# Optimization experiments

Measured on AMD Instinct MI355X. Metric: run time of the kernel, lower is better.

Reference implementation:

```python
import jax, jax.numpy as jnp
import numpy as np

# ---- straight-through binary quantizers (custom VJP matches torch autograd.Functions) ----
@jax.custom_vjp
def bq(x):
    return jnp.sign(x)
def _bq_fwd(x):
    return jnp.sign(x), x
def _bq_bwd(x, g):
    return (g * ((x > -1.0) & (x < 1.0)).astype(g.dtype),)
bq.defvjp(_bq_fwd, _bq_bwd)

@jax.custom_vjp
def bq_quad(x):
    return jnp.sign(x)
def _bqq_fwd(x):
    return jnp.sign(x), x
def _bqq_bwd(x, g):
    return (jnp.maximum(2.0 - jnp.abs(2.0 * x), 0.0) * g,)
bq_quad.defvjp(_bqq_fwd, _bqq_bwd)

def bilinear(x, W, s, b):
    # BiLinear: row-centered sign weights scaled by learned per-row factor, sign activations
    Wc = W - jnp.mean(W, axis=-1, keepdims=True)
    Wb = s * bq(Wc)                      # (out, in)
    return bq(x) @ Wb.T + b

def selective_scan(u, delta, A, Bs, Cs, D, delta_bias):
    # u, delta: (B,K,Dn,L); A: (K,Dn,N); Bs,Cs: (B,K,N,L); D, delta_bias: (K,Dn)
    Bn, K, Dn, L = u.shape
    N = A.shape[-1]
    delta = jax.nn.softplus(delta + delta_bias[None, :, :, None])
    def step(h, inp):
        ut, dt, Bt, Ct = inp             # (B,K,Dn),(B,K,Dn),(B,K,N),(B,K,N)
        dA = jnp.exp(dt[..., None] * A[None])
        h = dA * h + (dt * ut)[..., None] * Bt[:, :, None, :]
        y = jnp.einsum('bkdn,bkn->bkd', h, Ct)
        return h, y
    h0 = jnp.zeros((Bn, K, Dn, N), u.dtype)
    _, ys = jax.lax.scan(step, h0,
                         (u.transpose(3, 0, 1, 2), delta.transpose(3, 0, 1, 2),
                          Bs.transpose(3, 0, 1, 2), Cs.transpose(3, 0, 1, 2)))
    y = ys.transpose(1, 2, 3, 0)         # (B,K,Dn,L)
    return y + D[None, :, :, None] * u

def _forward(x, W_in, b_in, s_in, move0_b, conv_W, conv_b, rp_b0, prelu_a, rp_b1,
             Wl, bl, sl, Wd, bd, sd, dt_bias, A_logs, Ds, ln_w, ln_b, W_out, b_out, s_out):
    Bn, H, Wi, dm = x.shape
    Dn = conv_W.shape[0]
    K = 4
    N = A_logs.shape[1]
    R = Wd.shape[2]
    L = H * Wi
    xz = bilinear(x, W_in, s_in, b_in)                  # (B,H,W,2*Dn)
    xp, z = jnp.split(xz, 2, axis=-1)
    xc = xp.transpose(0, 3, 1, 2)                       # (B,Dn,H,W)
    # BConv2d: move0 bias -> sign (quad STE) -> binary conv -> RPReLU -> residual
    t = bq_quad(xc + move0_b[None, :, None, None])
    sc = jax.lax.stop_gradient(jnp.mean(jnp.abs(conv_W), axis=(1, 2, 3), keepdims=True))
    cw = jnp.clip(conv_W, -1.0, 1.0)
    Wb = jax.lax.stop_gradient(sc * jnp.sign(conv_W) - cw) + cw
    t = jax.lax.conv_general_dilated(t, Wb, (1, 1), [(1, 1), (1, 1)],
                                     dimension_numbers=('NCHW', 'OIHW', 'NCHW'))
    t = t + conv_b[None, :, None, None]
    t = t + rp_b0[None, :, None, None]
    t = jnp.where(t >= 0, t, prelu_a[None, :, None, None] * t)
    t = t + rp_b1[None, :, None, None] + xc
    xconv = jax.nn.silu(t)
    # 4-direction scan inputs
    x_flat = xconv.reshape(Bn, Dn, L)
    x_tr = xconv.transpose(0, 1, 3, 2).reshape(Bn, Dn, L)
    x_hwwh = jnp.stack([x_flat, x_tr], axis=1)
    xs = jnp.concatenate([x_hwwh, jnp.flip(x_hwwh, axis=-1)], axis=1)   # (B,K,Dn,L)
    # NOTE: torch does .view(B,L,-1) on contiguous (B,Dn,L) slices = raw reshape (not transpose)
    xin = xs.reshape(Bn, K, L, Dn)
    x_dbl = jax.vmap(bilinear, in_axes=(1, 0, 0, 0), out_axes=1)(xin, Wl, sl, bl)  # (B,K,L,R+2N)
    x_dbl = x_dbl.transpose(0, 1, 3, 2)                                 # (B,K,R+2N,L)
    dts_r, Bs, Cs = jnp.split(x_dbl, [R, R + N], axis=2)
    dts_in = dts_r.reshape(Bn, K, L, R)  # raw reshape, matches torch .view
    dts = jax.vmap(bilinear, in_axes=(1, 0, 0, 0), out_axes=1)(dts_in, Wd, sd, bd)  # (B,K,L,Dn)
    dts = dts.transpose(0, 1, 3, 2)                                     # (B,K,Dn,L)
    A = -jnp.exp(A_logs).reshape(K, Dn, N)
    out_y = selective_scan(xs, dts, A, Bs, Cs, Ds.reshape(K, Dn), dt_bias.reshape(K, Dn))
    inv_y = jnp.flip(out_y[:, 2:4], axis=-1)
    wh_y = out_y[:, 1].reshape(Bn, Dn, Wi, H).transpose(0, 1, 3, 2).reshape(Bn, Dn, L)
    invwh_y = inv_y[:, 1].reshape(Bn, Dn, Wi, H).transpose(0, 1, 3, 2).reshape(Bn, Dn, L)
    y = out_y[:, 0] + inv_y[:, 0] + wh_y + invwh_y                      # (B,Dn,L)
    y = y.transpose(0, 2, 1).reshape(Bn, H, Wi, Dn)
    mu = jnp.mean(y, axis=-1, keepdims=True)
    var = jnp.var(y, axis=-1, keepdims=True)
    y = (y - mu) / jnp.sqrt(var + 1e-5) * ln_w + ln_b                   # LayerNorm eps=1e-5
    y = y * jax.nn.silu(z)
    return bilinear(y, W_out, s_out, b_out)

def setup_inputs():
    key = jax.random.key(0)
    ks = jax.random.split(key, 12)
    B, H, Wi, dm = 4, 64, 64, 96
    Dn, N, R, K = 192, 16, 6, 4
    u = lambda k, sh, a: jax.random.uniform(k, sh, jnp.float32, -a, a)
    x = jax.random.normal(ks[0], (B, H, Wi, dm), jnp.float32)
    W_in = u(ks[1], (2 * Dn, dm), 0.015)
    b_in = u(ks[2], (2 * Dn,), 0.01)
    s_in = jnp.mean(jnp.abs(W_in), axis=1, keepdims=True)
    move0_b = jnp.zeros((Dn,), jnp.float32)
    conv_W = 0.05 * jax.random.normal(ks[3], (Dn, Dn, 3, 3), jnp.float32)
    conv_b = u(ks[4], (Dn,), 0.01)
    rp_b0 = jnp.zeros((Dn,), jnp.float32)
    prelu_a = 0.25 * jnp.ones((Dn,), jnp.float32)
    rp_b1 = jnp.zeros((Dn,), jnp.float32)
    Wl = u(ks[5], (K, R + 2 * N, Dn), 0.015)
    bl = u(ks[6], (K, R + 2 * N), 0.01)
    sl = jnp.mean(jnp.abs(Wl), axis=2, keepdims=True)
    std = R ** -0.5
    Wd = u(ks[7], (K, Dn, R), std)
    bd = u(ks[8], (K, Dn), 0.01)
    sd = jnp.mean(jnp.abs(Wd), axis=2, keepdims=True)
    dt = jnp.exp(jax.random.uniform(ks[9], (K * Dn,), jnp.float32)
                 * (np.log(0.1) - np.log(0.001)) + np.log(0.001))
    dt = jnp.clip(dt, 1e-4, None)
    dt_bias = dt + jnp.log(-jnp.expm1(-dt))
    A_logs = jnp.tile(jnp.log(jnp.arange(1, N + 1, dtype=jnp.float32))[None, :], (K * Dn, 1))
    Ds = jnp.ones((K * Dn,), jnp.float32)
    ln_w = jnp.ones((Dn,), jnp.float32)
    ln_b = jnp.zeros((Dn,), jnp.float32)
    W_out = u(ks[10], (dm, Dn), 0.015)
    b_out = u(ks[11], (dm,), 0.01)
    s_out = jnp.mean(jnp.abs(W_out), axis=1, keepdims=True)
    return dict(x=x, W_in=W_in, b_in=b_in, s_in=s_in, move0_b=move0_b, conv_W=conv_W,
                conv_b=conv_b, rp_b0=rp_b0, prelu_a=prelu_a, rp_b1=rp_b1, Wl=Wl, bl=bl,
                sl=sl, Wd=Wd, bd=bd, sd=sd, dt_bias=dt_bias, A_logs=A_logs, Ds=Ds,
                ln_w=ln_w, ln_b=ln_b, W_out=W_out, b_out=b_out, s_out=s_out)

def reference(x, W_in, b_in, s_in, move0_b, conv_W, conv_b, rp_b0, prelu_a, rp_b1,
              Wl, bl, sl, Wd, bd, sd, dt_bias, A_logs, Ds, ln_w, ln_b, W_out, b_out, s_out):
    return _forward(x, W_in, b_in, s_in, move0_b, conv_W, conv_b, rp_b0, prelu_a, rp_b1,
                    Wl, bl, sl, Wd, bd, sd, dt_bias, A_logs, Ds, ln_w, ln_b, W_out, b_out, s_out)
```

## Files before the change

kernel.cpp:

```cpp
#include <hip/hip_runtime.h>
#include <math.h>
#include <stdint.h>

#define BB 4
#define HH 64
#define WW2 64
#define DM 96
#define DN 192
#define KK 4
#define NN 16
#define RR 6
#define LL 4096
#define RN 38

#define LOG2E 1.4426950408889634f
#define LN2   0.6931471805599453f

#define OFF_WDB      0
#define OFF_WCS      4608
#define OFF_WAUX     15360
#define OFF_WSC      16896
#define OFF_WBIB     17088
#define OFF_WOUTB    18240
#define OFF_WLBB     18816
#define OFF_XBP      19728
#define OFF_PXS      19728
#define OFF_SSUM     19728
#define OFF_YB       19728
#define OFF_XC       412992
#define OFF_ZS       3558720
#define OFF_XCONV    6704448
#define OFF_XS       9850176
#define OFF_XDBL     22433088
#define OFF_HEND     OFF_XCONV

#define PLANE 4356

__device__ __forceinline__ float fsign(float v) {
  return (v > 0.f) ? 1.f : ((v < 0.f) ? -1.f : 0.f);
}
__device__ __forceinline__ float softplusf(float v) {
  return fmaxf(v, 0.f) + LN2 * log2f(1.f + exp2f(-fabsf(v) * LOG2E));
}
__device__ __forceinline__ float siluf(float v) {
  return v / (1.f + expf(-v));
}
__device__ __forceinline__ float waveAllSum(float s) {
  #pragma unroll
  for (int off = 32; off; off >>= 1) s += __shfl_xor(s, off, 64);
  return s;
}

__global__ __launch_bounds__(64) void k_prep(
    const float* __restrict__ W_in, const float* __restrict__ s_in,
    const float* __restrict__ W_out, const float* __restrict__ s_out,
    const float* __restrict__ Wl, const float* __restrict__ sl,
    const float* __restrict__ Wd, const float* __restrict__ sd,
    const float* __restrict__ convW, float* __restrict__ ws) {
  __shared__ float srow[1728];
  int r = blockIdx.x, lane = threadIdx.x;
  if (r < 384) {
    const float* row = W_in + r * DM;
    float s = 0.f;
    for (int c = lane; c < DM; c += 64) s += row[c];
    s = waveAllSum(s);
    float mean = s / (float)DM;
    if (lane < 3) {
      uint32_t wv = 0;
      #pragma unroll
      for (int i = 0; i < 32; ++i) wv |= (row[lane * 32 + i] - mean > 0.f ? 1u : 0u) << i;
      ((uint32_t*)(ws + OFF_WBIB))[r * 3 + lane] = wv;
    }
  } else if (r < 480) {
    int m = r - 384;
    const float* row = W_out + m * DN;
    float s = 0.f;
    for (int c = lane; c < DN; c += 64) s += row[c];
    s = waveAllSum(s);
    float mean = s / (float)DN;
    if (lane < 6) {
      uint32_t wv = 0;
      #pragma unroll
      for (int i = 0; i < 32; ++i) wv |= (row[lane * 32 + i] - mean > 0.f ? 1u : 0u) << i;
      ((uint32_t*)(ws + OFF_WOUTB))[m * 6 + lane] = wv;
    }
  } else if (r < 632) {
    int idx = r - 480;
    const float* row = Wl + idx * DN;
    float s = 0.f;
    for (int c = lane; c < DN; c += 64) s += row[c];
    s = waveAllSum(s);
    float mean = s / (float)DN;
    if (lane < 6) {
      uint32_t wv = 0;
      #pragma unroll
      for (int i = 0; i < 32; ++i) wv |= (row[lane * 32 + i] - mean > 0.f ? 1u : 0u) << i;
      ((uint32_t*)(ws + OFF_WLBB))[idx * 6 + lane] = wv;
    }
  } else if (r < 1400) {
    int idx = r - 632;
    const float* row = Wd + idx * RR;
    float s = (lane < RR) ? row[lane] : 0.f;
    s = waveAllSum(s);
    float mean = s / (float)RR;
    unsigned long long mb = __ballot((lane < RR) && (row[lane] - mean > 0.f));
    if (lane == 0) {
      ((uint32_t*)(ws + OFF_WDB))[idx] = (uint32_t)mb & 0x3Fu;
      (ws + OFF_WDB)[768 + idx] = sd[idx];
    }
  } else {
    int o = r - 1400;
    const float* row = convW + o * 1728;
    float s = 0.f;
    for (int j = lane; j < 1728; j += 64) {
      float v = row[j];
      srow[j] = v;
      s += fabsf(v);
    }
    s = waveAllSum(s);
    __syncthreads();
    float sc = s / 1728.f;
    uint32_t* wb = (uint32_t*)(ws + OFF_WCS);
    int* aux = (int*)(ws + OFF_WAUX);
    float* scf = ws + OFF_WSC;
    uint32_t word = 0;
    if (lane < 54) {
      int cw = lane / 9, tap = lane % 9;
      #pragma unroll
      for (int i = 0; i < 32; ++i)
        word |= (srow[(cw * 32 + i) * 9 + tap] > 0.f ? 1u : 0u) << i;
      wb[o * 56 + lane] = word;
    } else if (lane < 56) {
      wb[o * 56 + lane] = 0u;
    }
    int pc = (lane < 54) ? 2 * (int)__popc(word) - 32 : 0;
    int tapid = lane % 9;
    int wst = 0;
    #pragma unroll
    for (int cw = 0; cw < 6; ++cw) wst += __shfl(pc, cw * 9 + tapid, 64);
    int w_t[9];
    #pragma unroll
    for (int t9 = 0; t9 < 9; ++t9) w_t[t9] = __shfl(wst, t9, 64);
    if (lane == 0) {
      aux[o * 8 + 0] = w_t[0] + w_t[3] + w_t[6];
      aux[o * 8 + 1] = w_t[2] + w_t[5] + w_t[8];
      aux[o * 8 + 2] = w_t[0] + w_t[1] + w_t[2];
      aux[o * 8 + 3] = w_t[6] + w_t[7] + w_t[8];
      aux[o * 8 + 4] = w_t[0];
      aux[o * 8 + 5] = w_t[2];
      aux[o * 8 + 6] = w_t[6];
      aux[o * 8 + 7] = w_t[8];
      scf[o] = sc;
    }
  }
}

__global__ __launch_bounds__(384) void k_bilin_in(
    const float* __restrict__ x, const float* __restrict__ b_in,
    const float* __restrict__ s_in, const float* __restrict__ move0,
    const float* __restrict__ ws, float* __restrict__ xc, float* __restrict__ zs,
    uint32_t* __restrict__ xb) {
  __shared__ uint32_t spx[16 * 3];
  __shared__ float sxz[384 * 17];
  __shared__ float smv[DN];
  int p0 = blockIdx.x * 16;
  if (threadIdx.x < 48) {
    int pix = threadIdx.x / 3, wd = threadIdx.x % 3;
    const float* base = x + (size_t)(p0 + pix) * DM + wd * 32;
    uint32_t wv = 0;
    #pragma unroll
    for (int i = 0; i < 32; ++i) wv |= (base[i] > 0.f ? 1u : 0u) << i;
    spx[pix * 3 + wd] = wv;
  }
  if (threadIdx.x < DN) smv[threadIdx.x] = move0[threadIdx.x];
  __syncthreads();
  int o = threadIdx.x;
  uint32_t w0, w1, w2;
  {
    const uint32_t* wb = (const uint32_t*)(ws + OFF_WBIB) + o * 3;
    w0 = wb[0]; w1 = wb[1]; w2 = wb[2];
  }
  float bias = b_in[o], sc = s_in[o];
  #pragma unroll
  for (int pix = 0; pix < 16; ++pix) {
    int P = (int)__popc(spx[pix * 3 + 0] ^ w0) + (int)__popc(spx[pix * 3 + 1] ^ w1) +
            (int)__popc(spx[pix * 3 + 2] ^ w2);
    sxz[o * 17 + pix] = bias + sc * (float)(DM - 2 * P);
  }
  __syncthreads();
  int b = p0 >> 12, l0 = p0 & 4095;
  for (int f = threadIdx.x; f < DN * 16; f += 384) {
    int od = f >> 4, pix = f & 15;
    xc[((size_t)(b * DN + od)) * LL + l0 + pix] = sxz[od * 17 + pix];
  }
  for (int f = threadIdx.x; f < DN * 16; f += 384) {
    int pix = f / DN, oz = f - pix * DN;
    zs[(size_t)(p0 + pix) * DN + oz] = siluf(sxz[(DN + oz) * 17 + pix]);
  }
  if (threadIdx.x < 96) {
    int pix = threadIdx.x / 6, cw = threadIdx.x % 6;
    uint32_t wv = 0;
    #pragma unroll
    for (int i = 0; i < 32; ++i) {
      int dch = cw * 32 + i;
      wv |= ((sxz[dch * 17 + pix] + smv[dch] > 0.f) ? 1u : 0u) << i;
    }
    int l = l0 + pix, h = l >> 6, w = l & 63;
    uint32_t* plane = xb + (size_t)(b * 6 + cw) * PLANE;
    plane[(h + 1) * 66 + 1 + w] = wv;
  }
}

__global__ __launch_bounds__(256) void k_conv(
    const uint32_t* __restrict__ xb, const float* __restrict__ xc,
    const uint32_t* __restrict__ wbits, const int* __restrict__ aux,
    const float* __restrict__ scf, const float* __restrict__ conv_b,
    const float* __restrict__ rp_b0, const float* __restrict__ prelu_a,
    const float* __restrict__ rp_b1, float* __restrict__ xconv) {
  int og = blockIdx.x & 3;
  int stripe = (blockIdx.x >> 2) & 15;
  int b = blockIdx.x >> 6;
  int w = threadIdx.x & 63, r = threadIdx.x >> 6;
  int h = stripe * 4 + r;

  __shared__ uint32_t swb[48 * 56];
  __shared__ int saux[48 * 8];
  __shared__ float sconst[48 * 4];
  for (int i = threadIdx.x; i < 48 * 56; i += 256) swb[i] = wbits[og * (48 * 56) + i];
  for (int i = threadIdx.x; i < 48 * 8; i += 256) saux[i] = aux[og * (48 * 8) + i];
  if (threadIdx.x < 48) {
    int o = og * 48 + threadIdx.x;
    sconst[threadIdx.x * 4 + 0] = scf[o];
    sconst[threadIdx.x * 4 + 1] = conv_b[o] + rp_b0[o];
    sconst[threadIdx.x * 4 + 2] = prelu_a[o];
    sconst[threadIdx.x * 4 + 3] = rp_b1[o];
  }

  uint32_t xw[6][9];
  const uint32_t* xpb = xb + (size_t)b * 6 * PLANE;
  #pragma unroll
  for (int cw = 0; cw < 6; ++cw) {
    const uint32_t* plane = xpb + cw * PLANE + (h + 1) * 66 + (w + 1);
    #pragma unroll
    for (int dy = 0; dy < 3; ++dy) {
      #pragma unroll
      for (int dx = 0; dx < 3; ++dx)
        xw[cw][dy * 3 + dx] = plane[(dy - 1) * 66 + (dx - 1)];
    }
  }
  bool isL = (w == 0), isR = (w == 63);
  bool isT = (h == 0), isB = (h == 63);
  const float* xcp = xc + ((size_t)(b * DN + og * 48)) * LL + h * 64 + w;
  float* xop = xconv + ((size_t)(b * DN + og * 48)) * LL + h * 64 + w;
  __syncthreads();

  #pragma unroll 1
  for (int oc = 0; oc < 48; ++oc) {
    const uint32_t* wp = &swb[oc * 56];
    int P = 0;
    #pragma unroll
    for (int cw = 0; cw < 6; ++cw) {
      int pp = 0;
      #pragma unroll
      for (int t = 0; t < 9; ++t) pp += (int)__popc(wp[cw * 9 + t] ^ xw[cw][t]);
      P += pp;
    }
    int corr = isL ? saux[oc * 8 + 0] : (isR ? saux[oc * 8 + 1] : 0);
    if (isT) {
      corr += saux[oc * 8 + 2];
      if (isL) corr -= saux[oc * 8 + 4];
      if (isR) corr -= saux[oc * 8 + 5];
    }
    if (isB) {
      corr += saux[oc * 8 + 3];
      if (isL) corr -= saux[oc * 8 + 6];
      if (isR) corr -= saux[oc * 8 + 7];
    }
    float acc = sconst[oc * 4 + 0] * (float)(1728 - 2 * P + corr);
    float t = acc + sconst[oc * 4 + 1];
    t = (t >= 0.f) ? t : sconst[oc * 4 + 2] * t;
    t += sconst[oc * 4 + 3] + *xcp;
    *xop = siluf(t);
    xcp += LL; xop += LL;
  }
}

__global__ __launch_bounds__(256) void k_build_xs(const float* __restrict__ xconv,
                                                  float* __restrict__ xs,
                                                  uint32_t* __restrict__ pxs) {
  __shared__ float tile[64][65];
  int bd = blockIdx.x;
  int b = bd / DN, d = bd % DN;
  const float* img = xconv + (size_t)bd * LL;
  for (int i = threadIdx.x; i < LL; i += 256)
    tile[i >> 6][i & 63] = img[i];
  __syncthreads();
  int lane = threadIdx.x & 63;
  #pragma unroll
  for (int k = 0; k < 4; ++k) {
    size_t base = ((size_t)((b * KK + k) * DN + d)) * LL;
    for (int j = threadIdx.x; j < LL; j += 256) {
      float v;
      if (k == 0)      v = tile[j >> 6][j & 63];
      else if (k == 1) v = tile[j & 63][j >> 6];
      else if (k == 2) { int t2 = 4095 - j; v = tile[t2 >> 6][t2 & 63]; }
      else             { int t2 = 4095 - j; v = tile[t2 & 63][t2 >> 6]; }
      xs[base + j] = v;
      unsigned long long m = __ballot(v > 0.f);
      if (lane == 0)       pxs[(base + j) >> 5] = (uint32_t)m;
      else if (lane == 32) pxs[(base + j) >> 5] = (uint32_t)(m >> 32);
    }
  }
}

__global__ __launch_bounds__(256) void k_xdbl(
    const uint32_t* __restrict__ pxs, const float* __restrict__ ws,
    const float* __restrict__ bl, const float* __restrict__ sl,
    float* __restrict__ xdbl) {
  int bk = blockIdx.x >> 4;
  int l = ((blockIdx.x & 15) << 8) + threadIdx.x;
  int k = bk & 3;
  __shared__ uint32_t swl[RN * 6];
  __shared__ float sbias[RN], ssc[RN];
  if (threadIdx.x < RN * 6) swl[threadIdx.x] = ((const uint32_t*)(ws + OFF_WLBB))[k * RN * 6 + threadIdx.x];
  if (threadIdx.x < RN) {
    sbias[threadIdx.x] = bl[k * RN + threadIdx.x];
    ssc[threadIdx.x] = sl[k * RN + threadIdx.x];
  }
  uint32_t xb[6];
  const uint32_t* pp = pxs + (size_t)bk * 24576 + (size_t)l * 6;
  #pragma unroll
  for (int j = 0; j < 6; ++j) xb[j] = pp[j];
  __syncthreads();
  float* xo = xdbl + (size_t)bk * (RN * LL) + l;
  #pragma unroll 1
  for (int o = 0; o < RN; ++o) {
    int P = 0;
    #pragma unroll
    for (int j = 0; j < 6; ++j) P += (int)__popc(xb[j] ^ swl[o * 6 + j]);
    xo[(size_t)o * LL] = sbias[o] + ssc[o] * (float)(DN - 2 * P);
  }
}

__device__ __forceinline__ void rpowers(float r, float* a) {
  float r2 = r * r, r3 = r2 * r, r4 = r2 * r2, r8 = r4 * r4;
  a[0] = r;       a[1] = r2;      a[2] = r3;      a[3] = r4;
  a[4] = r4 * r;  a[5] = r4 * r2; a[6] = r4 * r3; a[7] = r8;
  a[8] = r8 * r;  a[9] = r8 * r2; a[10] = r8 * r3; a[11] = r8 * r4;
  a[12] = r8 * a[4]; a[13] = r8 * a[5]; a[14] = r8 * a[6]; a[15] = r8 * r8;
}

__global__ __launch_bounds__(192) void k_scan_a(
    const float* __restrict__ xs, const float* __restrict__ xdbl,
    const float* __restrict__ ws, const float* __restrict__ bd,
    const float* __restrict__ dt_bias, const float* __restrict__ A_logs,
    float* __restrict__ hend, float* __restrict__ Ssum) {
  int c = blockIdx.x & 63;
  int bk = blockIdx.x >> 6;
  int k = bk & 3;
  int d = threadIdx.x;
  int t0 = c << 6;
  __shared__ uint32_t sdtm[64];
  __shared__ float4 sB4[256];
  __shared__ float sDV[7 * 192], sR[7 * 192];
  float* sBf = (float*)sB4;
  const float* dtbase = xdbl + (size_t)bk * (RN * LL);
  if (d < 64) {
    const float2* p2 = (const float2*)(dtbase + t0 * 6 + d * 6);
    float2 a = p2[0], bb = p2[1], cc = p2[2];
    uint32_t m = (a.x > 0.f ? 1u : 0u) | (a.y > 0.f ? 2u : 0u) |
                 (bb.x > 0.f ? 4u : 0u) | (bb.y > 0.f ? 8u : 0u) |
                 (cc.x > 0.f ? 16u : 0u) | (cc.y > 0.f ? 32u : 0u);
    sdtm[d] = m;
  }
  {
    const float4* Bp = (const float4*)(xdbl + ((size_t)bk * RN + RR) * LL);
    for (int i = d; i < 256; i += 192) {
      int n = i >> 4, j = i & 15;
      float4 v = Bp[n * 1024 + (t0 >> 2) + j];
      sBf[(4 * j + 0) * 16 + n] = v.x;
      sBf[(4 * j + 1) * 16 + n] = v.y;
      sBf[(4 * j + 2) * 16 + n] = v.z;
      sBf[(4 * j + 3) * 16 + n] = v.w;
    }
  }
  uint32_t w6 = ((const uint32_t*)(ws + OFF_WDB))[k * DN + d];
  float sdv = (ws + OFF_WDB)[768 + k * DN + d];
  float biasd = bd[k * DN + d] + dt_bias[k * DN + d];
  #pragma unroll
  for (int pc = 0; pc < 7; ++pc) {
    float dv = softplusf(biasd + sdv * (float)(RR - 2 * pc));
    sDV[pc * 192 + d] = dv;
    sR[pc * 192 + d] = exp2f(-dv * LOG2E);
  }
  float Araw[16];
  bool fok = true;
  {
    const float* ap = A_logs + (k * DN + d) * NN;
    #pragma unroll
    for (int n = 0; n < NN; ++n) {
      Araw[n] = -expf(ap[n]);
      fok = fok && (fabsf(Araw[n] + (float)(n + 1)) < 1e-3f);
    }
  }
  bool fastpath = (__ballot(fok) == ~0ull);
  float h[16];
  #pragma unroll
  for (int n = 0; n < NN; ++n) h[n] = 0.f;
  float S = 0.f;
  const float* up = xs + ((size_t)bk * DN + d) * LL + t0;
  __syncthreads();
  if (fastpath) {
    #pragma unroll 1
    for (int tt = 0; tt < 16; ++tt) {
      float4 u4 = *(const float4*)(up + 4 * tt);
      #pragma unroll
      for (int q = 0; q < 4; ++q) {
        int t = 4 * tt + q;
        float uv = (q == 0) ? u4.x : (q == 1) ? u4.y : (q == 2) ? u4.z : u4.w;
        int pc = (int)__popc(sdtm[t] ^ w6);
        float dv = sDV[pc * 192 + d];
        float rr = sR[pc * 192 + d];
        S += dv;
        float du = dv * uv;
        float a[16];
        rpowers(rr, a);
        #pragma unroll
        for (int g = 0; g < 4; ++g) {
          float4 bv = sB4[t * 4 + g];
          h[4 * g + 0] = a[4 * g + 0] * h[4 * g + 0] + du * bv.x;
          h[4 * g + 1] = a[4 * g + 1] * h[4 * g + 1] + du * bv.y;
          h[4 * g + 2] = a[4 * g + 2] * h[4 * g + 2] + du * bv.z;
          h[4 * g + 3] = a[4 * g + 3] * h[4 * g + 3] + du * bv.w;
        }
      }
    }
  } else {
    float An[16];
    #pragma unroll
    for (int n = 0; n < NN; ++n) An[n] = Araw[n] * LOG2E;
    #pragma unroll 1
    for (int tt = 0; tt < 16; ++tt) {
      float4 u4 = *(const float4*)(up + 4 * tt);
      #pragma unroll
      for (int q = 0; q < 4; ++q) {
        int t = 4 * tt + q;
        float uv = (q == 0) ? u4.x : (q == 1) ? u4.y : (q == 2) ? u4.z : u4.w;
        int pc = (int)__popc(sdtm[t] ^ w6);
        float dv = sDV[pc * 192 + d];
        S += dv;
        float du = dv * uv;
        #pragma unroll
        for (int g = 0; g < 4; ++g) {
          float4 bv = sB4[t * 4 + g];
          float a0 = exp2f(dv * An[4 * g + 0]);
          float a1 = exp2f(dv * An[4 * g + 1]);
          float a2 = exp2f(dv * An[4 * g + 2]);
          float a3 = exp2f(dv * An[4 * g + 3]);
          h[4 * g + 0] = a0 * h[4 * g + 0] + du * bv.x;
          h[4 * g + 1] = a1 * h[4 * g + 1] + du * bv.y;
          h[4 * g + 2] = a2 * h[4 * g + 2] + du * bv.z;
          h[4 * g + 3] = a3 * h[4 * g + 3] + du * bv.w;
        }
      }
    }
  }
  float* hp = hend + (size_t)c * 49152 + (size_t)(bk * DN + d) * 16;
  #pragma unroll
  for (int n = 0; n < NN; n += 4)
    *(float4*)(hp + n) = make_float4(h[n], h[n + 1], h[n + 2], h[n + 3]);
  Ssum[c * 3072 + bk * DN + d] = S;
}

__global__ __launch_bounds__(256) void k_scan_b(
    const float* __restrict__ A_logs, const float* __restrict__ Ssum,
    float* __restrict__ hend) {
  int tid = blockIdx.x * 256 + threadIdx.x;
  int bkd = tid >> 4, n = tid & 15;
  int bk = bkd / DN, d = bkd - bk * DN;
  int k = bk & 3;
  float An2 = -expf(A_logs[(k * DN + d) * NN + n]) * LOG2E;
  float h = 0.f;
  float Sc = Ssum[bkd];
  float he = hend[tid];
  #pragma unroll 1
  for (int c = 0; c < 64; ++c) {
    float Sn = 0.f, hn = 0.f;
    if (c < 63) {
      Sn = Ssum[(c + 1) * 3072 + bkd];
      hn = hend[(size_t)(c + 1) * 49152 + tid];
    }
    hend[(size_t)c * 49152 + tid] = h;
    h = exp2f(An2 * Sc) * h + he;
    Sc = Sn; he = hn;
  }
}

__global__ __launch_bounds__(192) void k_scan_c(
    const float* __restrict__ xs, const float* __restrict__ xdbl,
    const float* __restrict__ ws, const float* __restrict__ bd,
    const float* __restrict__ dt_bias, const float* __restrict__ A_logs,
    const float* __restrict__ Ds, const float* __restrict__ h0buf,
    float* __restrict__ y) {
  int c = blockIdx.x & 63;
  int bk = blockIdx.x >> 6;
  int k = bk & 3;
  int d = threadIdx.x;
  int t0 = c << 6;
  __shared__ uint32_t sdtm[64];
  __shared__ float4 sB4[256];
  __shared__ float4 sC4[256];
  __shared__ float sDV[7 * 192], sR[7 * 192];
  float* sBf = (float*)sB4;
  float* sCf = (float*)sC4;
  const float* dtbase = xdbl + (size_t)bk * (RN * LL);
  if (d < 64) {
    const float2* p2 = (const float2*)(dtbase + t0 * 6 + d * 6);
    float2 a = p2[0], bb = p2[1], cc = p2[2];
    uint32_t m = (a.x > 0.f ? 1u : 0u) | (a.y > 0.f ? 2u : 0u) |
                 (bb.x > 0.f ? 4u : 0u) | (bb.y > 0.f ? 8u : 0u) |
                 (cc.x > 0.f ? 16u : 0u) | (cc.y > 0.f ? 32u : 0u);
    sdtm[d] = m;
  }
  {
    const float4* Bp = (const float4*)(xdbl + ((size_t)bk * RN + RR) * LL);
    const float4* Cp = (const float4*)(xdbl + ((size_t)bk * RN + RR + NN) * LL);
    for (int i = d; i < 256; i += 192) {
      int n = i >> 4, j = i & 15;
      float4 v = Bp[n * 1024 + (t0 >> 2) + j];
      sBf[(4 * j + 0) * 16 + n] = v.x;
      sBf[(4 * j + 1) * 16 + n] = v.y;
      sBf[(4 * j + 2) * 16 + n] = v.z;
      sBf[(4 * j + 3) * 16 + n] = v.w;
      float4 w = Cp[n * 1024 + (t0 >> 2) + j];
      sCf[(4 * j + 0) * 16 + n] = w.x;
      sCf[(4 * j + 1) * 16 + n] = w.y;
      sCf[(4 * j + 2) * 16 + n] = w.z;
      sCf[(4 * j + 3) * 16 + n] = w.w;
    }
  }
  uint32_t w6 = ((const uint32_t*)(ws + OFF_WDB))[k * DN + d];
  float sdv = (ws + OFF_WDB)[768 + k * DN + d];
  float biasd = bd[k * DN + d] + dt_bias[k * DN + d];
  float Dd = Ds[k * DN + d];
  #pragma unroll
  for (int pc = 0; pc < 7; ++pc) {
    float dv = softplusf(biasd + sdv * (float)(RR - 2 * pc));
    sDV[pc * 192 + d] = dv;
    sR[pc * 192 + d] = exp2f(-dv * LOG2E);
  }
  float Araw[16];
  bool fok = true;
  {
    const float* ap = A_logs + (k * DN + d) * NN;
    #pragma unroll
    for (int n = 0; n < NN; ++n) {
      Araw[n] = -expf(ap[n]);
      fok = fok && (fabsf(Araw[n] + (float)(n + 1)) < 1e-3f);
    }
  }
  bool fastpath = (__ballot(fok) == ~0ull);
  float h[16];
  {
    const float* hp = h0buf + (size_t)c * 49152 + (size_t)(bk * DN + d) * 16;
    #pragma unroll
    for (int n = 0; n < NN; n += 4) {
      float4 v = *(const float4*)(hp + n);
      h[n] = v.x; h[n + 1] = v.y; h[n + 2] = v.z; h[n + 3] = v.w;
    }
  }
  const float* up = xs + ((size_t)bk * DN + d) * LL + t0;
  float* yb = y + (size_t)(bk >> 2) * (LL * DN);
  __syncthreads();
  if (fastpath) {
    #pragma unroll 1
    for (int tt = 0; tt < 16; ++tt) {
      float4 u4 = *(const float4*)(up + 4 * tt);
      #pragma unroll
      for (int q = 0; q < 4; ++q) {
        int t = 4 * tt + q;
        float uv = (q == 0) ? u4.x : (q == 1) ? u4.y : (q == 2) ? u4.z : u4.w;
        int pc = (int)__popc(sdtm[t] ^ w6);
        float dv = sDV[pc * 192 + d];
        float rr = sR[pc * 192 + d];
        float du = dv * uv;
        float yv = Dd * uv;
        float a[16];
        rpowers(rr, a);
        #pragma unroll
        for (int g = 0; g < 4; ++g) {
          float4 bv = sB4[t * 4 + g];
          float4 cv = sC4[t * 4 + g];
          h[4 * g + 0] = a[4 * g + 0] * h[4 * g + 0] + du * bv.x;
          h[4 * g + 1] = a[4 * g + 1] * h[4 * g + 1] + du * bv.y;
          h[4 * g + 2] = a[4 * g + 2] * h[4 * g + 2] + du * bv.z;
          h[4 * g + 3] = a[4 * g + 3] * h[4 * g + 3] + du * bv.w;
          yv += cv.x * h[4 * g + 0];
          yv += cv.y * h[4 * g + 1];
          yv += cv.z * h[4 * g + 2];
          yv += cv.w * h[4 * g + 3];
        }
        int ta = t0 + t, l;
        if (k == 0)      l = ta;
        else if (k == 1) l = ((ta & 63) << 6) | (ta >> 6);
        else if (k == 2) l = 4095 - ta;
        else { int t2 = 4095 - ta; l = ((t2 & 63) << 6) | (t2 >> 6); }
        atomicAdd(&yb[(size_t)l * DN + d], yv);
      }
    }
  } else {
    float An[16];
    #pragma unroll
    for (int n = 0; n < NN; ++n) An[n] = Araw[n] * LOG2E;
    #pragma unroll 1
    for (int tt = 0; tt < 16; ++tt) {
      float4 u4 = *(const float4*)(up + 4 * tt);
      #pragma unroll
      for (int q = 0; q < 4; ++q) {
        int t = 4 * tt + q;
        float uv = (q == 0) ? u4.x : (q == 1) ? u4.y : (q == 2) ? u4.z : u4.w;
        int pc = (int)__popc(sdtm[t] ^ w6);
        float dv = sDV[pc * 192 + d];
        float du = dv * uv;
        float yv = Dd * uv;
        #pragma unroll
        for (int g = 0; g < 4; ++g) {
          float4 bv = sB4[t * 4 + g];
          float4 cv = sC4[t * 4 + g];
          float a0 = exp2f(dv * An[4 * g + 0]);
          float a1 = exp2f(dv * An[4 * g + 1]);
          float a2 = exp2f(dv * An[4 * g + 2]);
          float a3 = exp2f(dv * An[4 * g + 3]);
          h[4 * g + 0] = a0 * h[4 * g + 0] + du * bv.x;
          h[4 * g + 1] = a1 * h[4 * g + 1] + du * bv.y;
          h[4 * g + 2] = a2 * h[4 * g + 2] + du * bv.z;
          h[4 * g + 3] = a3 * h[4 * g + 3] + du * bv.w;
          yv += cv.x * h[4 * g + 0];
          yv += cv.y * h[4 * g + 1];
          yv += cv.z * h[4 * g + 2];
          yv += cv.w * h[4 * g + 3];
        }
        int ta = t0 + t, l;
        if (k == 0)      l = ta;
        else if (k == 1) l = ((ta & 63) << 6) | (ta >> 6);
        else if (k == 2) l = 4095 - ta;
        else { int t2 = 4095 - ta; l = ((t2 & 63) << 6) | (t2 >> 6); }
        atomicAdd(&yb[(size_t)l * DN + d], yv);
      }
    }
  }
}

__global__ __launch_bounds__(256) void k_ln(
    const float* __restrict__ y, const float* __restrict__ zs,
    const float* __restrict__ ln_w, const float* __restrict__ ln_b,
    uint32_t* __restrict__ ybits) {
  __shared__ float ty[64 * 193];
  __shared__ float ps[256];
  __shared__ float smu[64], srs[64];
  __shared__ float slw[DN], slb[DN];
  int b = blockIdx.x >> 6;
  int l0 = (blockIdx.x & 63) << 6;
  const float* yp = y + (size_t)(b * LL + l0) * DN;
  if (threadIdx.x < DN) {
    slw[threadIdx.x] = ln_w[threadIdx.x];
    slb[threadIdx.x] = ln_b[threadIdx.x];
  }
  {
    int lc = threadIdx.x / DN, d2 = threadIdx.x - lc * DN;
    for (int i = threadIdx.x; i < 64 * DN; i += 256) {
      ty[lc * 193 + d2] = yp[i];
      d2 += 256;
      if (d2 >= DN) { d2 -= DN; lc += 1; if (d2 >= DN) { d2 -= DN; lc += 1; } }
    }
  }
  __syncthreads();
  int lc = threadIdx.x & 63, part = threadIdx.x >> 6;
  float s = 0.f;
  for (int d = part * 48; d < part * 48 + 48; ++d) s += ty[lc * 193 + d];
  ps[threadIdx.x] = s;
  __syncthreads();
  if (threadIdx.x < 64)
    smu[threadIdx.x] = (ps[threadIdx.x] + ps[threadIdx.x + 64] +
                        ps[threadIdx.x + 128] + ps[threadIdx.x + 192]) / (float)DN;
  __syncthreads();
  float mu = smu[lc];
  float q = 0.f;
  for (int d = part * 48; d < part * 48 + 48; ++d) {
    float v = ty[lc * 193 + d] - mu; q += v * v;
  }
  ps[threadIdx.x] = q;
  __syncthreads();
  if (threadIdx.x < 64) {
    float var = (ps[threadIdx.x] + ps[threadIdx.x + 64] +
                 ps[threadIdx.x + 128] + ps[threadIdx.x + 192]) / (float)DN;
    srs[threadIdx.x] = rsqrtf(var + 1e-5f);
  }
  __syncthreads();
  for (int item = threadIdx.x; item < 64 * 6; item += 256) {
    int lc2 = item / 6, wd = item % 6;
    float mu2 = smu[lc2], rs2 = srs[lc2];
    const float* zb = zs + (size_t)(b * LL + l0 + lc2) * DN + wd * 32;
    uint32_t wv = 0;
    #pragma unroll
    for (int i = 0; i < 32; ++i) {
      int d = wd * 32 + i;
      float ln = (ty[lc2 * 193 + d] - mu2) * rs2 * slw[d] + slb[d];
      wv |= ((ln * zb[i] > 0.f) ? 1u : 0u) << i;
    }
    ybits[(size_t)(b * LL + l0 + lc2) * 6 + wd] = wv;
  }
}

__global__ __launch_bounds__(256) void k_out(
    const uint32_t* __restrict__ ybits, const float* __restrict__ ws,
    const float* __restrict__ b_out, const float* __restrict__ s_out,
    float* __restrict__ out) {
  __shared__ uint32_t sy[64 * 6];
  __shared__ uint32_t swo[96 * 6];
  __shared__ float sb[96], ssc[96];
  int p0 = blockIdx.x * 64;
  for (int i = threadIdx.x; i < 64 * 6; i += 256) sy[i] = ybits[(size_t)p0 * 6 + i];
  for (int i = threadIdx.x; i < 96 * 6; i += 256) swo[i] = ((const uint32_t*)(ws + OFF_WOUTB))[i];
  if (threadIdx.x < 96) {
    sb[threadIdx.x] = b_out[threadIdx.x];
    ssc[threadIdx.x] = s_out[threadIdx.x];
  }
  __syncthreads();
  for (int oi = threadIdx.x; oi < 64 * DM; oi += 256) {
    int pr = oi / DM, m = oi % DM;
    int P = 0;
    #pragma unroll
    for (int j = 0; j < 6; ++j) P += (int)__popc(sy[pr * 6 + j] ^ swo[m * 6 + j]);
    out[(size_t)(p0 + pr) * DM + m] = sb[m] + ssc[m] * (float)(DN - 2 * P);
  }
}

extern "C" void kernel_launch(void* const* d_in, const int* in_sizes, int n_in,
                              void* d_out, int out_size, void* d_ws, size_t ws_size,
                              hipStream_t stream) {
  const float* x       = (const float*)d_in[0];
  const float* W_in    = (const float*)d_in[1];
  const float* b_in    = (const float*)d_in[2];
  const float* s_in    = (const float*)d_in[3];
  const float* move0_b = (const float*)d_in[4];
  const float* conv_W  = (const float*)d_in[5];
  const float* conv_b  = (const float*)d_in[6];
  const float* rp_b0   = (const float*)d_in[7];
  const float* prelu_a = (const float*)d_in[8];
  const float* rp_b1   = (const float*)d_in[9];
  const float* Wl      = (const float*)d_in[10];
  const float* bl      = (const float*)d_in[11];
  const float* sl      = (const float*)d_in[12];
  const float* Wd      = (const float*)d_in[13];
  const float* bd      = (const float*)d_in[14];
  const float* sd      = (const float*)d_in[15];
  const float* dt_bias = (const float*)d_in[16];
  const float* A_logs  = (const float*)d_in[17];
  const float* Ds      = (const float*)d_in[18];
  const float* ln_w    = (const float*)d_in[19];
  const float* ln_b    = (const float*)d_in[20];
  const float* W_out   = (const float*)d_in[21];
  const float* b_out   = (const float*)d_in[22];
  const float* s_out   = (const float*)d_in[23];
  float* ws  = (float*)d_ws;
  float* out = (float*)d_out;

  hipLaunchKernelGGL(k_prep, dim3(1592), dim3(64), 0, stream,
                     W_in, s_in, W_out, s_out, Wl, sl, Wd, sd, conv_W, ws);
  hipMemsetAsync((void*)(ws + OFF_XBP), 0, (size_t)(4 * 6 * PLANE) * 4, stream);
  hipLaunchKernelGGL(k_bilin_in, dim3(1024), dim3(384), 0, stream,
                     x, b_in, s_in, move0_b, ws, ws + OFF_XC, ws + OFF_ZS,
                     (uint32_t*)(ws + OFF_XBP));
  hipLaunchKernelGGL(k_conv, dim3(256), dim3(256), 0, stream,
                     (const uint32_t*)(ws + OFF_XBP), ws + OFF_XC,
                     (const uint32_t*)(ws + OFF_WCS), (const int*)(ws + OFF_WAUX),
                     ws + OFF_WSC, conv_b, rp_b0, prelu_a, rp_b1,
                     ws + OFF_XCONV);
  hipLaunchKernelGGL(k_build_xs, dim3(768), dim3(256), 0, stream,
                     ws + OFF_XCONV, ws + OFF_XS, (uint32_t*)(ws + OFF_PXS));
  hipLaunchKernelGGL(k_xdbl, dim3(256), dim3(256), 0, stream,
                     (const uint32_t*)(ws + OFF_PXS), ws, bl, sl, ws + OFF_XDBL);
  hipLaunchKernelGGL(k_scan_a, dim3(1024), dim3(192), 0, stream,
                     ws + OFF_XS, ws + OFF_XDBL, ws, bd, dt_bias, A_logs,
                     ws + OFF_HEND, ws + OFF_SSUM);
  hipLaunchKernelGGL(k_scan_b, dim3(192), dim3(256), 0, stream,
                     A_logs, ws + OFF_SSUM, ws + OFF_HEND);
  hipMemsetAsync((void*)(ws + OFF_XC), 0, (size_t)3145728 * sizeof(float), stream);
  hipLaunchKernelGGL(k_scan_c, dim3(1024), dim3(192), 0, stream,
                     ws + OFF_XS, ws + OFF_XDBL, ws, bd, dt_bias, A_logs, Ds,
                     ws + OFF_HEND, ws + OFF_XC);
  hipLaunchKernelGGL(k_ln, dim3(256), dim3(256), 0, stream,
                     ws + OFF_XC, ws + OFF_ZS, ln_w, ln_b, (uint32_t*)(ws + OFF_YB));
  hipLaunchKernelGGL(k_out, dim3(256), dim3(256), 0, stream,
                     (const uint32_t*)(ws + OFF_YB), ws, b_out, s_out, out);
}
```

Measured before the change: 327.1 us.

## Replace scan atomics with in-place tile writes and a separate direction-combine kernel

The scan kernel no longer atomically adds each direction's output into a zeroed (L,D) buffer. Instead it stages outputs in a shared tile and writes them in place over its xs input. A new kernel then sums the four directional outputs with the required transposes and flips, producing a (B,D,L) layout, and the layernorm load is adapted to read that layout. This removes the memset and the scattered atomic traffic, at the cost of an extra kernel launch, a full extra read/write pass, and extra barriers inside the scan.

Measured after the change: 322.1 us. About the same (-1.5%).

```diff
diff --git a/kernel.cpp b/kernel.cpp
--- a/kernel.cpp
+++ b/kernel.cpp
@@ -497,11 +497,10 @@
 }
 
 __global__ __launch_bounds__(192) void k_scan_c(
-    const float* __restrict__ xs, const float* __restrict__ xdbl,
+    float* __restrict__ xs, const float* __restrict__ xdbl,
     const float* __restrict__ ws, const float* __restrict__ bd,
     const float* __restrict__ dt_bias, const float* __restrict__ A_logs,
-    const float* __restrict__ Ds, const float* __restrict__ h0buf,
-    float* __restrict__ y) {
+    const float* __restrict__ Ds, const float* __restrict__ h0buf) {
   int c = blockIdx.x & 63;
   int bk = blockIdx.x >> 6;
   int k = bk & 3;
@@ -511,6 +510,7 @@
   __shared__ float4 sB4[256];
   __shared__ float4 sC4[256];
   __shared__ float sDV[7 * 192], sR[7 * 192];
+  __shared__ float ytile[192 * 17];
   float* sBf = (float*)sB4;
   float* sCf = (float*)sC4;
   const float* dtbase = xdbl + (size_t)bk * (RN * LL);
@@ -569,85 +569,94 @@
       h[n] = v.x; h[n + 1] = v.y; h[n + 2] = v.z; h[n + 3] = v.w;
     }
   }
-  const float* up = xs + ((size_t)bk * DN + d) * LL + t0;
-  float* yb = y + (size_t)(bk >> 2) * (LL * DN);
-  __syncthreads();
-  if (fastpath) {
+  float* xbase = xs + ((size_t)bk * DN) * LL;
+  const float* up = xbase + (size_t)d * LL + t0;
+  float An[16];
+  if (!fastpath) {
+    #pragma unroll
+    for (int n = 0; n < NN; ++n) An[n] = Araw[n] * LOG2E;
+  }
+  __syncthreads();
+  #pragma unroll 1
+  for (int seg = 0; seg < 4; ++seg) {
     #pragma unroll 1
-    for (int tt = 0; tt < 16; ++tt) {
-      float4 u4 = *(const float4*)(up + 4 * tt);
+    for (int tt = 0; tt < 4; ++tt) {
+      float4 u4 = *(const float4*)(up + seg * 16 + 4 * tt);
       #pragma unroll
       for (int q = 0; q < 4; ++q) {
-        int t = 4 * tt + q;
-        float uv = (q == 0) ? u4.x : (q == 1) ? u4.y : (q == 2) ? u4.z : u4.w;
-        int pc = (int)__popc(sdtm[t] ^ w6);
-        float dv = sDV[pc * 192 + d];
-        float rr = sR[pc * 192 + d];
-        float du = dv * uv;
-        float yv = Dd * uv;
-        float a[16];
-        rpowers(rr, a);
-        #pragma unroll
-        for (int g = 0; g < 4; ++g) {
-          float4 bv = sB4[t * 4 + g];
-          float4 cv = sC4[t * 4 + g];
-          h[4 * g + 0] = a[4 * g + 0] * h[4 * g + 0] + du * bv.x;
-          h[4 * g + 1] = a[4 * g + 1] * h[4 * g + 1] + du * bv.y;
-          h[4 * g + 2] = a[4 * g + 2] * h[4 * g + 2] + du * bv.z;
-          h[4 * g + 3] = a[4 * g + 3] * h[4 * g + 3] + du * bv.w;
-          yv += cv.x * h[4 * g + 0];
-          yv += cv.y * h[4 * g + 1];
-          yv += cv.z * h[4 * g + 2];
-          yv += cv.w * h[4 * g + 3];
-        }
-        int ta = t0 + t, l;
-        if (k == 0)      l = ta;
-        else if (k == 1) l = ((ta & 63) << 6) | (ta >> 6);
-        else if (k == 2) l = 4095 - ta;
-        else { int t2 = 4095 - ta; l = ((t2 & 63) << 6) | (t2 >> 6); }
-        atomicAdd(&yb[(size_t)l * DN + d], yv);
-      }
-    }
-  } else {
-    float An[16];
-    #pragma unroll
-    for (int n = 0; n < NN; ++n) An[n] = Araw[n] * LOG2E;
-    #pragma unroll 1
-    for (int tt = 0; tt < 16; ++tt) {
-      float4 u4 = *(const float4*)(up + 4 * tt);
-      #pragma unroll
-      for (int q = 0; q < 4; ++q) {
-        int t = 4 * tt + q;
+        int t = seg * 16 + 4 * tt + q;
         float uv = (q == 0) ? u4.x : (q == 1) ? u4.y : (q == 2) ? u4.z : u4.w;
         int pc = (int)__popc(sdtm[t] ^ w6);
         float dv = sDV[pc * 192 + d];
         float du = dv * uv;
         float yv = Dd * uv;
-        #pragma unroll
-        for (int g = 0; g < 4; ++g) {
-          float4 bv = sB4[t * 4 + g];
-          float4 cv = sC4[t * 4 + g];
-          float a0 = exp2f(dv * An[4 * g + 0]);
-          float a1 = exp2f(dv * An[4 * g + 1]);
-          float a2 = exp2f(dv * An[4 * g + 2]);
-          float a3 = exp2f(dv * An[4 * g + 3]);
-          h[4 * g + 0] = a0 * h[4 * g + 0] + du * bv.x;
-          h[4 * g + 1] = a1 * h[4 * g + 1] + du * bv.y;
-          h[4 * g + 2] = a2 * h[4 * g + 2] + du * bv.z;
-          h[4 * g + 3] = a3 * h[4 * g + 3] + du * bv.w;
-          yv += cv.x * h[4 * g + 0];
-          yv += cv.y * h[4 * g + 1];
-          yv += cv.z * h[4 * g + 2];
-          yv += cv.w * h[4 * g + 3];
+        if (fastpath) {
+          float rr = sR[pc * 192 + d];
+          float a[16];
+          rpowers(rr, a);
+          #pragma unroll
+          for (int g = 0; g < 4; ++g) {
+            float4 bv = sB4[t * 4 + g];
+            float4 cv = sC4[t * 4 + g];
+            h[4 * g + 0] = a[4 * g + 0] * h[4 * g + 0] + du * bv.x;
+            h[4 * g + 1] = a[4 * g + 1] * h[4 * g + 1] + du * bv.y;
+            h[4 * g + 2] = a[4 * g + 2] * h[4 * g + 2] + du * bv.z;
+            h[4 * g + 3] = a[4 * g + 3] * h[4 * g + 3] + du * bv.w;
+            yv += cv.x * h[4 * g + 0];
+            yv += cv.y * h[4 * g + 1];
+            yv += cv.z * h[4 * g + 2];
+            yv += cv.w * h[4 * g + 3];
+          }
+        } else {
+          #pragma unroll
+          for (int g = 0; g < 4; ++g) {
+            float4 bv = sB4[t * 4 + g];
+            float4 cv = sC4[t * 4 + g];
+            float a0 = exp2f(dv * An[4 * g + 0]);
+            float a1 = exp2f(dv * An[4 * g + 1]);
+            float a2 = exp2f(dv * An[4 * g + 2]);
+            float a3 = exp2f(dv * An[4 * g + 3]);
+            h[4 * g + 0] = a0 * h[4 * g + 0] + du * bv.x;
+            h[4 * g + 1] = a1 * h[4 * g + 1] + du * bv.y;
+            h[4 * g + 2] = a2 * h[4 * g + 2] + du * bv.z;
+            h[4 * g + 3] = a3 * h[4 * g + 3] + du * bv.w;
+            yv += cv.x * h[4 * g + 0];
+            yv += cv.y * h[4 * g + 1];
+            yv += cv.z * h[4 * g + 2];
+            yv += cv.w * h[4 * g + 3];
+          }
         }
-        int ta = t0 + t, l;
-        if (k == 0)      l = ta;
-        else if (k == 1) l = ((ta & 63) << 6) | (ta >> 6);
-        else if (k == 2) l = 4095 - ta;
-        else { int t2 = 4095 - ta; l = ((t2 & 63) << 6) | (t2 >> 6); }
-        atomicAdd(&yb[(size_t)l * DN + d], yv);
+        ytile[d * 17 + (t & 15)] = yv;
       }
     }
+    __syncthreads();
+    for (int i = d; i < 3072; i += 192) {
+      int dd = i >> 4, tq = i & 15;
+      xbase[(size_t)dd * LL + t0 + seg * 16 + tq] = ytile[dd * 17 + tq];
+    }
+    __syncthreads();
+  }
+}
+
+__global__ __launch_bounds__(256) void k_comb(const float* __restrict__ xs,
+                                              float* __restrict__ y) {
+  __shared__ float tA[64][65], tB[64][65];
+  int bd = blockIdx.x;
+  int b = bd / DN, d = bd % DN;
+  const float* p0 = xs + ((size_t)((b * 4 + 0) * DN + d)) * LL;
+  const float* p1 = xs + ((size_t)((b * 4 + 1) * DN + d)) * LL;
+  const float* p2 = xs + ((size_t)((b * 4 + 2) * DN + d)) * LL;
+  const float* p3 = xs + ((size_t)((b * 4 + 3) * DN + d)) * LL;
+  for (int i = threadIdx.x; i < LL; i += 256) {
+    tA[i >> 6][i & 63] = p1[i];
+    tB[i >> 6][i & 63] = p3[i];
+  }
+  __syncthreads();
+  float* yo = y + (size_t)bd * LL;
+  for (int l = threadIdx.x; l < LL; l += 256) {
+    float v = p0[l] + tA[l & 63][l >> 6] + p2[4095 - l] +
+              tB[63 - (l & 63)][63 - (l >> 6)];
+    yo[l] = v;
   }
 }
 
@@ -661,18 +670,14 @@
   __shared__ float slw[DN], slb[DN];
   int b = blockIdx.x >> 6;
   int l0 = (blockIdx.x & 63) << 6;
-  const float* yp = y + (size_t)(b * LL + l0) * DN;
+  const float* yp = y + (size_t)b * DN * LL + l0;
   if (threadIdx.x < DN) {
     slw[threadIdx.x] = ln_w[threadIdx.x];
     slb[threadIdx.x] = ln_b[threadIdx.x];
   }
-  {
-    int lc = threadIdx.x / DN, d2 = threadIdx.x - lc * DN;
-    for (int i = threadIdx.x; i < 64 * DN; i += 256) {
-      ty[lc * 193 + d2] = yp[i];
-      d2 += 256;
-      if (d2 >= DN) { d2 -= DN; lc += 1; if (d2 >= DN) { d2 -= DN; lc += 1; } }
-    }
+  for (int i = threadIdx.x; i < 64 * DN; i += 256) {
+    int d2 = i >> 6, lc = i & 63;
+    ty[lc * 193 + d2] = yp[(size_t)d2 * LL + lc];
   }
   __syncthreads();
   int lc = threadIdx.x & 63, part = threadIdx.x >> 6;
@@ -786,10 +791,11 @@
                      ws + OFF_HEND, ws + OFF_SSUM);
   hipLaunchKernelGGL(k_scan_b, dim3(192), dim3(256), 0, stream,
                      A_logs, ws + OFF_SSUM, ws + OFF_HEND);
-  hipMemsetAsync((void*)(ws + OFF_XC), 0, (size_t)3145728 * sizeof(float), stream);
   hipLaunchKernelGGL(k_scan_c, dim3(1024), dim3(192), 0, stream,
                      ws + OFF_XS, ws + OFF_XDBL, ws, bd, dt_bias, A_logs, Ds,
-                     ws + OFF_HEND, ws + OFF_XC);
+                     ws + OFF_HEND);
+  hipLaunchKernelGGL(k_comb, dim3(768), dim3(256), 0, stream,
+                     ws + OFF_XS, ws + OFF_XC);
   hipLaunchKernelGGL(k_ln, dim3(256), dim3(256), 0, stream,
                      ws + OFF_XC, ws + OFF_ZS, ln_w, ln_b, (uint32_t*)(ws + OFF_YB));
   hipLaunchKernelGGL(k_out, dim3(256), dim3(256), 0, stream,
```
